# Kernel optimization log

Measured on AMD Instinct MI355X. Metric: run time of the kernel, lower is better.

Reference implementation:

```python
import jax, jax.numpy as jnp
import numpy as np

N = 50000   # total residue nodes across the batch of peptides
E = 800000  # total directed intra-peptide edges (avg degree 16)
D = 512


def _w(k, shape):
    fan_in = shape[0]
    return (jax.random.normal(k, shape, jnp.float32) / np.sqrt(fan_in)).astype(jnp.float32)


def setup_inputs() -> dict:
    key = jax.random.key(0)
    ks = jax.random.split(key, 12)
    return {
        "peptide_feature": jax.random.normal(ks[0], (N, D), jnp.float32),
        "edge_index": jax.random.randint(ks[1], (2, E), 0, N),
        # aanet_proj: 512 -> 1024 -> 1024 -> 512 -> 80 (ReLU between, none after last)
        "W1": _w(ks[2], (512, 1024)), "b1": jnp.zeros((1024,), jnp.float32),
        "W2": _w(ks[3], (1024, 1024)), "b2": jnp.zeros((1024,), jnp.float32),
        "W3": _w(ks[4], (1024, 512)), "b3": jnp.zeros((512,), jnp.float32),
        "W4": _w(ks[5], (512, 80)), "b4": jnp.zeros((80,), jnp.float32),
        # in_net: 80 -> 512
        "Win": _w(ks[6], (80, 512)), "bin_": jnp.zeros((512,), jnp.float32),
        # GIN conv MLP: 512 -> 512 -> 512 (eps = 0)
        "Wg1": _w(ks[7], (512, 512)), "bg1": jnp.zeros((512,), jnp.float32),
        "Wg2": _w(ks[8], (512, 512)), "bg2": jnp.zeros((512,), jnp.float32),
        # out_net: 512 -> 80
        "Wout": _w(ks[9], (512, 80)), "bout": jnp.zeros((80,), jnp.float32),
    }


def reference(peptide_feature, edge_index, W1, b1, W2, b2, W3, b3, W4, b4,
              Win, bin_, Wg1, bg1, Wg2, bg2, Wout, bout):
    relu = jax.nn.relu
    # aanet_proj
    h = relu(peptide_feature @ W1 + b1)
    h = relu(h @ W2 + b2)
    h = relu(h @ W3 + b3)
    peptide_feat = h @ W4 + b4                      # [N, 80]
    # in_net
    x = peptide_feat @ Win + bin_                   # [N, 512]
    # GIN message passing (sum aggregation, eps=0): per-sample loop in the
    # original is equivalent to one global pass since edges are sample-local.
    src, dst = edge_index[0], edge_index[1]
    agg = jax.ops.segment_sum(x[src], dst, num_segments=N)   # [N, 512]
    g = x + agg
    g = relu(g @ Wg1 + bg1) @ Wg2 + bg2             # GIN MLP
    # out_net
    peptide_mask = g @ Wout + bout                  # [N, 80]
    return peptide_mask, peptide_feat
```

## Files before the change

kernel.cpp:

```cpp
#include <hip/hip_runtime.h>
#include <stdint.h>


using bf16x8 = __attribute__((ext_vector_type(8))) short;
using f32x4  = __attribute__((ext_vector_type(4))) float;

__device__ inline unsigned short f2bf(float f) {
    union { float f; unsigned u; } v; v.f = f;
    unsigned u = v.u;
    u += 0x7FFFu + ((u >> 16) & 1u);
    return (unsigned short)(u >> 16);
}
__device__ inline float bf2f(unsigned u16) {
    return __uint_as_float(u16 << 16);
}

struct PreDescs {
    const float* W[8]; unsigned short* Wt[8];
    int K[8], M[8], Kp[8], ntx[8], start[8];
    int tEnd, cEnd, eEnd;
    const float* feat; unsigned short* featb; int nFeat;
    const int* ei; int E; int* cnt;
};

__global__ __launch_bounds__(256) void rg_preprocess(PreDescs d) {
    int b = blockIdx.x;
    int tid = threadIdx.x;
    if (b < d.tEnd) {
        __shared__ float t[32][33];
        int di = 0;
#pragma unroll
        for (int i = 1; i < 8; ++i) if (b >= d.start[i]) di = i;
        int local = b - d.start[di];
        int bx = local % d.ntx[di];
        int by = local / d.ntx[di];
        const float* W = d.W[di];
        unsigned short* Wt = d.Wt[di];
        int K = d.K[di], M = d.M[di], Kp = d.Kp[di];
        int mb = bx * 32, kb = by * 32;
        int tx = tid & 31, tg = tid >> 5;
#pragma unroll
        for (int p = 0; p < 4; ++p) {
            int r = tg + p * 8;
            int k = kb + r, m = mb + tx;
            t[r][tx] = (k < K && m < M) ? W[(size_t)k * M + m] : 0.f;
        }
        __syncthreads();
#pragma unroll
        for (int p = 0; p < 4; ++p) {
            int r = tg + p * 8;
            int mo = mb + r, ko = kb + tx;
            Wt[(size_t)mo * Kp + ko] = f2bf(t[tx][r]);
        }
    } else if (b < d.cEnd) {
        int i = ((b - d.tEnd) * 256 + tid) * 4;
        if (i + 3 < d.nFeat) {
            float4 v = *(const float4*)(d.feat + i);
            ushort4 o; o.x = f2bf(v.x); o.y = f2bf(v.y); o.z = f2bf(v.z); o.w = f2bf(v.w);
            *(ushort4*)(d.featb + i) = o;
        }
    } else {
        int e = (b - d.cEnd) * 256 + tid;
        if (e < d.E) atomicAdd(&d.cnt[d.ei[d.E + e]], 1);
    }
}

template <bool RELU, bool OUT_BF, bool OUT_F32, bool DEGB, int MT>
__device__ __forceinline__ void gemm_body(
    int bid,
    const unsigned short* __restrict__ A, const unsigned short* __restrict__ Bt,
    const float* __restrict__ bias, const int* __restrict__ deg, int Mvalid,
    unsigned short* __restrict__ outB, float* __restrict__ outF,
    int Nrows, int Kp, int Mp, int gN)
{
    __shared__ __align__(16) unsigned short As[128 * 64];
    __shared__ __align__(16) unsigned short Bs[128 * 64];

    int xcd = bid & 7;
    int slot = bid >> 3;
    int c = slot % MT;
    int rsub = slot / MT;
    int rt = rsub * 8 + xcd;
    if (rt >= gN) return;
    const int rowBase = rt * 128;
    const int nBase   = c * 128;

    const int tid  = threadIdx.x;
    const int lane = tid & 63;
    const int w    = tid >> 6;
    const int wm   = w & 1, wn = w >> 1;

    f32x4 acc[4][4];
#pragma unroll
    for (int i = 0; i < 4; ++i)
#pragma unroll
        for (int j = 0; j < 4; ++j) acc[i][j] = (f32x4){0.f, 0.f, 0.f, 0.f};

    const int nkt = Kp >> 6;
    for (int kt = 0; kt < nkt; ++kt) {
        __syncthreads();
        const int k0 = kt * 64;
#pragma unroll
        for (int i = 0; i < 4; ++i) {
            int q   = i * 256 + tid;
            int r   = q >> 3;
            int cbg = (q & 7) ^ (r & 7);
            const unsigned short* gp = A + (size_t)(rowBase + r) * Kp + k0 + cbg * 8;
            __builtin_amdgcn_global_load_lds(
                (const __attribute__((address_space(1))) void*)gp,
                (__attribute__((address_space(3))) void*)(&As[q * 8]), 16, 0, 0);
        }
#pragma unroll
        for (int i = 0; i < 4; ++i) {
            int q   = i * 256 + tid;
            int r   = q >> 3;
            int cbg = (q & 7) ^ (r & 7);
            const unsigned short* gp = Bt + (size_t)(nBase + r) * Kp + k0 + cbg * 8;
            __builtin_amdgcn_global_load_lds(
                (const __attribute__((address_space(1))) void*)gp,
                (__attribute__((address_space(3))) void*)(&Bs[q * 8]), 16, 0, 0);
        }
        __syncthreads();
#pragma unroll
        for (int kk = 0; kk < 2; ++kk) {
            bf16x8 a[4], b[4];
            const int cb = kk * 4 + (lane >> 4);
#pragma unroll
            for (int i = 0; i < 4; ++i) {
                int r = wm * 64 + i * 16 + (lane & 15);
                a[i] = *(const bf16x8*)&As[(r * 8 + (cb ^ (r & 7))) * 8];
            }
#pragma unroll
            for (int j = 0; j < 4; ++j) {
                int r = wn * 64 + j * 16 + (lane & 15);
                b[j] = *(const bf16x8*)&Bs[(r * 8 + (cb ^ (r & 7))) * 8];
            }
#pragma unroll
            for (int i = 0; i < 4; ++i)
#pragma unroll
                for (int j = 0; j < 4; ++j)
                    acc[i][j] = __builtin_amdgcn_mfma_f32_16x16x32_bf16(b[j], a[i], acc[i][j], 0, 0, 0);
        }
    }

    const int quad = lane >> 4;
#pragma unroll
    for (int i = 0; i < 4; ++i) {
        int row = rowBase + wm * 64 + i * 16 + (lane & 15);
        if (row >= Nrows) continue;
        float sc = 1.f;
        if (DEGB) sc = 1.f + (float)deg[row];
#pragma unroll
        for (int j = 0; j < 4; ++j) {
            int colb = nBase + wn * 64 + j * 16 + quad * 4;
            float4 bv = (colb < Mvalid) ? *(const float4*)(bias + colb)
                                        : (float4){0.f, 0.f, 0.f, 0.f};
            float v0 = acc[i][j][0] + sc * bv.x;
            float v1 = acc[i][j][1] + sc * bv.y;
            float v2 = acc[i][j][2] + sc * bv.z;
            float v3 = acc[i][j][3] + sc * bv.w;
            if (RELU) {
                v0 = v0 > 0.f ? v0 : 0.f; v1 = v1 > 0.f ? v1 : 0.f;
                v2 = v2 > 0.f ? v2 : 0.f; v3 = v3 > 0.f ? v3 : 0.f;
            }
            if (OUT_BF) {
                ushort4 o; o.x = f2bf(v0); o.y = f2bf(v1); o.z = f2bf(v2); o.w = f2bf(v3);
                *(ushort4*)(outB + (size_t)row * Mp + colb) = o;
            }
            if (OUT_F32) {
                if (colb < Mvalid)
                    *(float4*)(outF + (size_t)row * Mvalid + colb) = (float4){v0, v1, v2, v3};
            }
        }
    }
}

template <bool RELU, bool OUT_BF, bool OUT_F32, bool DEGB, int MT>
__global__ __launch_bounds__(256) void rg_gemm(
    const unsigned short* __restrict__ A, const unsigned short* __restrict__ Bt,
    const float* __restrict__ bias, const int* __restrict__ deg, int Mvalid,
    unsigned short* __restrict__ outB, float* __restrict__ outF,
    int Nrows, int Kp, int Mp, int gN)
{
    gemm_body<RELU, OUT_BF, OUT_F32, DEGB, MT>(blockIdx.x, A, Bt, bias, deg,
                                               Mvalid, outB, outF, Nrows, Kp, Mp, gN);
}

template <bool RELU, int MT>
__device__ __forceinline__ void gemm256_body(
    int bid,
    const unsigned short* __restrict__ A, const unsigned short* __restrict__ Bt,
    const float* __restrict__ bias, unsigned short* __restrict__ outB,
    int Nrows, int NrowsPad, int Kp, int Mp, int gN2)
{
    __shared__ __align__(16) unsigned short As[2][2][128 * 64];
    __shared__ __align__(16) unsigned short Bs[2][2][128 * 64];

    int xcd = bid & 7;
    int slotb = bid >> 3;
    int c = slotb % MT;
    int rsub = slotb / MT;
    int rt = rsub * 8 + xcd;
    if (rt >= gN2) return;
    const int rowBase = rt * 256;
    const int nBase   = c * 256;

    const int tid  = threadIdx.x;
    const int lane = tid & 63;
    const int w    = tid >> 6;
    const int wm   = w & 1;
    const int wn   = w >> 1;

    f32x4 acc[8][4];
#pragma unroll
    for (int i = 0; i < 8; ++i)
#pragma unroll
        for (int j = 0; j < 4; ++j) acc[i][j] = (f32x4){0.f, 0.f, 0.f, 0.f};

    const int nkt = Kp >> 6;

    auto stageA = [&](int t, int hf) {
        const int k0 = t << 6;
        unsigned short* dst = &As[t & 1][hf][0];
#pragma unroll
        for (int ld = 0; ld < 2; ++ld) {
            int q   = ld * 512 + tid;
            int r   = q >> 3;
            int cbg = (q & 7) ^ (r & 7);
            int grow = rowBase + hf * 128 + r;
            grow = grow < NrowsPad ? grow : NrowsPad - 1;
            const unsigned short* gp = A + (size_t)grow * Kp + k0 + cbg * 8;
            __builtin_amdgcn_global_load_lds(
                (const __attribute__((address_space(1))) void*)gp,
                (__attribute__((address_space(3))) void*)(dst + q * 8), 16, 0, 0);
        }
    };
    auto stageB = [&](int t, int hf) {
        const int k0 = t << 6;
        unsigned short* dst = &Bs[t & 1][hf][0];
#pragma unroll
        for (int ld = 0; ld < 2; ++ld) {
            int q   = ld * 512 + tid;
            int r   = q >> 3;
            int cbg = (q & 7) ^ (r & 7);
            const unsigned short* gp = Bt + (size_t)(nBase + hf * 128 + r) * Kp + k0 + cbg * 8;
            __builtin_amdgcn_global_load_lds(
                (const __attribute__((address_space(1))) void*)gp,
                (__attribute__((address_space(3))) void*)(dst + q * 8), 16, 0, 0);
        }
    };

    auto phase = [&](int a, int q, int mh, int nh) {
        const int slot = a & 1;
        bf16x8 av[4][2], bv[2][2];
#pragma unroll
        for (int i = 0; i < 4; ++i) {
            int lr = wm * 64 + i * 16 + (lane & 15);
#pragma unroll
            for (int kk = 0; kk < 2; ++kk) {
                int cb = kk * 4 + (lane >> 4);
                av[i][kk] = *(const bf16x8*)&As[slot][mh][(lr * 8 + (cb ^ (lr & 7))) * 8];
            }
        }
#pragma unroll
        for (int j = 0; j < 2; ++j) {
            int lr = wn * 32 + j * 16 + (lane & 15);
#pragma unroll
            for (int kk = 0; kk < 2; ++kk) {
                int cb = kk * 4 + (lane >> 4);
                bv[j][kk] = *(const bf16x8*)&Bs[slot][nh][(lr * 8 + (cb ^ (lr & 7))) * 8];
            }
        }
        if (q == 0) { if (a + 1 < nkt) stageA(a + 1, 1); }
        if (q == 1) { if (a + 1 < nkt) stageB(a + 1, 1); }
        if (q == 2) { if (a + 2 < nkt) stageA(a + 2, 0); }
        if (q == 3) {
            if (a + 2 < nkt) {
                stageB(a + 2, 0);
                asm volatile("s_waitcnt vmcnt(4)" ::: "memory");
            } else if (a + 1 < nkt) {
                asm volatile("s_waitcnt vmcnt(0)" ::: "memory");
            }
        }
        __builtin_amdgcn_sched_barrier(0);
        __builtin_amdgcn_s_barrier();
        asm volatile("s_waitcnt lgkmcnt(0)" ::: "memory");
        __builtin_amdgcn_sched_barrier(0);
        __builtin_amdgcn_s_setprio(1);
#pragma unroll
        for (int i = 0; i < 4; ++i)
#pragma unroll
            for (int j = 0; j < 2; ++j)
#pragma unroll
                for (int kk = 0; kk < 2; ++kk)
                    acc[mh * 4 + i][nh * 2 + j] = __builtin_amdgcn_mfma_f32_16x16x32_bf16(
                        bv[j][kk], av[i][kk], acc[mh * 4 + i][nh * 2 + j], 0, 0, 0);
        __builtin_amdgcn_s_setprio(0);
        __builtin_amdgcn_sched_barrier(0);
        __builtin_amdgcn_s_barrier();
    };

    stageA(0, 0); stageB(0, 0); stageA(0, 1); stageB(0, 1);
    stageA(1, 0); stageB(1, 0);
    asm volatile("s_waitcnt vmcnt(4)" ::: "memory");
    __builtin_amdgcn_sched_barrier(0);
    __builtin_amdgcn_s_barrier();
    __builtin_amdgcn_sched_barrier(0);

    for (int a = 0; a < nkt; ++a) {
        phase(a, 0, 0, 0);
        phase(a, 1, 0, 1);
        phase(a, 2, 1, 0);
        phase(a, 3, 1, 1);
    }

    const int quad = lane >> 4;
#pragma unroll
    for (int mi = 0; mi < 8; ++mi) {
        int row = rowBase + ((mi >> 2) * 2 + wm) * 64 + (mi & 3) * 16 + (lane & 15);
        if (row >= Nrows) continue;
#pragma unroll
        for (int nj = 0; nj < 4; ++nj) {
            int colb = nBase + (nj >> 1) * 128 + wn * 32 + (nj & 1) * 16 + quad * 4;
            float4 bvv = *(const float4*)(bias + colb);
            float v0 = acc[mi][nj][0] + bvv.x;
            float v1 = acc[mi][nj][1] + bvv.y;
            float v2 = acc[mi][nj][2] + bvv.z;
            float v3 = acc[mi][nj][3] + bvv.w;
            if (RELU) {
                v0 = v0 > 0.f ? v0 : 0.f; v1 = v1 > 0.f ? v1 : 0.f;
                v2 = v2 > 0.f ? v2 : 0.f; v3 = v3 > 0.f ? v3 : 0.f;
            }
            ushort4 o; o.x = f2bf(v0); o.y = f2bf(v1); o.z = f2bf(v2); o.w = f2bf(v3);
            *(ushort4*)(outB + (size_t)row * Mp + colb) = o;
        }
    }
}

template <bool RELU, int MT>
__global__ __launch_bounds__(512) void rg_gemm256(
    const unsigned short* __restrict__ A, const unsigned short* __restrict__ Bt,
    const float* __restrict__ bias, unsigned short* __restrict__ outB,
    int Nrows, int NrowsPad, int Kp, int Mp, int gN2)
{
    gemm256_body<RELU, MT>(blockIdx.x, A, Bt, bias, outB, Nrows, NrowsPad, Kp, Mp, gN2);
}

__global__ __launch_bounds__(512) void rg_gemm256_l1_scatter(
    const unsigned short* __restrict__ A, const unsigned short* __restrict__ Bt,
    const float* __restrict__ bias, unsigned short* __restrict__ outB,
    int Nrows, int NrowsPad, int Kp, int Mp, int gN2,
    int gemmBlocks, const int* __restrict__ ei, int E,
    int* __restrict__ cursor, int* __restrict__ cols)
{
    int bid = blockIdx.x;
    if (bid < gemmBlocks) {
        gemm256_body<true, 4>(bid, A, Bt, bias, outB, Nrows, NrowsPad, Kp, Mp, gN2);
    } else {
        int e = (bid - gemmBlocks) * 512 + threadIdx.x;
        if (e < E) {
            int d = ei[E + e];
            int p = atomicAdd(&cursor[d], 1);
            cols[p] = ei[e];
        }
    }
}

__device__ __forceinline__ void rg_gridbar(int* bar, int nb, int phase) {
    __syncthreads();
    if (threadIdx.x == 0) {
        __threadfence();
        atomicAdd(bar, 1);
        int target = phase * nb;
        while (__hip_atomic_load(bar, __ATOMIC_RELAXED, __HIP_MEMORY_SCOPE_AGENT) < target) {}
        __threadfence();
    }
    __syncthreads();
}

__global__ __launch_bounds__(1024) void rg_scan_all(
    const int* __restrict__ cnt, int* __restrict__ rowptr, int* __restrict__ cursor,
    int* __restrict__ bsums, int* bar, int Nn, int E, int nb)
{
    __shared__ int sd[1024];
    const int tid = threadIdx.x;
    const int bid = blockIdx.x;
    const int i   = bid * 1024 + tid;

    int v = (i < Nn) ? cnt[i] : 0;
    sd[tid] = v;
    __syncthreads();
    for (int off = 1; off < 1024; off <<= 1) {
        int t = (tid >= off) ? sd[tid - off] : 0;
        __syncthreads();
        sd[tid] += t;
        __syncthreads();
    }
    if (tid == 1023) bsums[bid] = sd[1023];
    rg_gridbar(bar, nb, 1);

    if (bid == 0 && tid < 64) {
        int bv = (tid < nb) ? bsums[tid] : 0;
        int incl = bv;
#pragma unroll
        for (int off = 1; off < 64; off <<= 1) {
            int t = __shfl_up(incl, off, 64);
            if (tid >= off) incl += t;
        }
        if (tid < nb) bsums[tid] = incl - bv;
    }
    rg_gridbar(bar, nb, 2);

    if (i < Nn) {
        int ex = sd[tid] - v + bsums[bid];
        rowptr[i] = ex; cursor[i] = ex;
    }
    if (i == 0) rowptr[Nn] = E;
}

__global__ __launch_bounds__(256) void rg_agg80(
    const unsigned short* __restrict__ pf, const int* __restrict__ rowptr,
    const int* __restrict__ cols, unsigned short* __restrict__ s, int Nn)
{
    int node = blockIdx.x * 4 + (threadIdx.x >> 6);
    if (node >= Nn) return;
    int lane = threadIdx.x & 63;
    const unsigned* xp = (const unsigned*)pf;
    size_t off = (size_t)node * 64 + lane;
    unsigned u = xp[off];
    float a0 = bf2f(u & 0xffffu), a1 = bf2f(u >> 16);
    int beg = rowptr[node], end = rowptr[node + 1];
    int e = beg;
    for (; e + 8 <= end; e += 8) {
        unsigned v[8];
#pragma unroll
        for (int t = 0; t < 8; ++t) v[t] = xp[(size_t)cols[e + t] * 64 + lane];
#pragma unroll
        for (int t = 0; t < 8; ++t) { a0 += bf2f(v[t] & 0xffffu); a1 += bf2f(v[t] >> 16); }
    }
    for (; e < end; ++e) {
        unsigned v = xp[(size_t)cols[e] * 64 + lane];
        a0 += bf2f(v & 0xffffu); a1 += bf2f(v >> 16);
    }
    unsigned o = (unsigned)f2bf(a0) | ((unsigned)f2bf(a1) << 16);
    ((unsigned*)s)[off] = o;
}

extern "C" void kernel_launch(void* const* d_in, const int* in_sizes, int n_in,
                              void* d_out, int out_size, void* d_ws, size_t ws_size,
                              hipStream_t stream)
{
    const float* feat = (const float*)d_in[0];
    const int*   ei   = (const int*)d_in[1];
    const float* W1 = (const float*)d_in[2];  const float* b1 = (const float*)d_in[3];
    const float* W2 = (const float*)d_in[4];  const float* b2 = (const float*)d_in[5];
    const float* W3 = (const float*)d_in[6];  const float* b3 = (const float*)d_in[7];
    const float* W4 = (const float*)d_in[8];  const float* b4 = (const float*)d_in[9];
    const float* Wi = (const float*)d_in[10]; const float* bi = (const float*)d_in[11];
    const float* Wg1 = (const float*)d_in[12]; const float* bg1 = (const float*)d_in[13];
    const float* Wg2 = (const float*)d_in[14]; const float* bg2 = (const float*)d_in[15];
    const float* Wo = (const float*)d_in[16]; const float* bo = (const float*)d_in[17];

    const int N = in_sizes[0] / 512;
    const int E = in_sizes[1] / 2;
    const int gN = (N + 127) / 128;
    const int Npad = gN * 128;

    char* ws = (char*)d_ws;
    size_t o = 0;
    auto alloc = [&](size_t bytes) { char* p = ws + o; o += (bytes + 255) & ~(size_t)255; return p; };
    unsigned short* bufA = (unsigned short*)alloc((size_t)Npad * 1024 * 2);
    unsigned short* bufB = (unsigned short*)alloc((size_t)Npad * 1024 * 2);
    unsigned short* bufC = (unsigned short*)alloc((size_t)Npad * 512 * 2);
    unsigned short* W1t = (unsigned short*)alloc((size_t)1024 * 512 * 2);
    unsigned short* W2t = (unsigned short*)alloc((size_t)1024 * 1024 * 2);
    unsigned short* W3t = (unsigned short*)alloc((size_t)512 * 1024 * 2);
    unsigned short* W4t = (unsigned short*)alloc((size_t)128 * 512 * 2);
    unsigned short* Wit = (unsigned short*)alloc((size_t)512 * 128 * 2);
    unsigned short* Wg1t = (unsigned short*)alloc((size_t)512 * 512 * 2);
    unsigned short* Wg2t = (unsigned short*)alloc((size_t)512 * 512 * 2);
    unsigned short* Wot = (unsigned short*)alloc((size_t)128 * 512 * 2);
    int* cnt    = (int*)alloc((size_t)(N + 64) * 4);
    int* bar    = cnt + N;
    int* rowptr = (int*)alloc((size_t)(N + 1) * 4);
    int* cursor = (int*)alloc((size_t)N * 4);
    int* cols   = (int*)alloc((size_t)E * 4);
    int* bsums  = (int*)alloc(256);

    float* out_mask = (float*)d_out;
    float* out_feat = (float*)d_out + (size_t)N * 80;

    hipMemsetAsync(cnt, 0, (size_t)(N + 64) * 4, stream);
    {
        PreDescs d;
        const float* Ws[8]  = {W1, W2, W3, W4, Wi, Wg1, Wg2, Wo};
        unsigned short* Ts[8] = {W1t, W2t, W3t, W4t, Wit, Wg1t, Wg2t, Wot};
        int Ks[8]  = {512, 1024, 1024, 512, 80, 512, 512, 512};
        int Ms[8]  = {1024, 1024, 512, 80, 512, 512, 512, 80};
        int Kps[8] = {512, 1024, 1024, 512, 128, 512, 512, 512};
        int Mps[8] = {1024, 1024, 512, 128, 512, 512, 512, 128};
        int st = 0;
        for (int i = 0; i < 8; ++i) {
            d.W[i] = Ws[i]; d.Wt[i] = Ts[i];
            d.K[i] = Ks[i]; d.M[i] = Ms[i]; d.Kp[i] = Kps[i];
            d.ntx[i] = Mps[i] / 32;
            d.start[i] = st;
            st += (Mps[i] / 32) * (Kps[i] / 32);
        }
        d.tEnd = st;
        d.cEnd = st + (N * 512) / 1024;
        d.eEnd = d.cEnd + (E + 255) / 256;
        d.feat = feat; d.featb = bufC; d.nFeat = N * 512;
        d.ei = ei; d.E = E; d.cnt = cnt;
        rg_preprocess<<<d.eEnd, 256, 0, stream>>>(d);
    }

    const int nb = (N + 1023) / 1024;
    rg_scan_all<<<nb, 1024, 0, stream>>>(cnt, rowptr, cursor, bsums, bar, N, E, nb);

    const int rg8 = ((gN + 7) / 8) * 8;
    auto grid = [&](int MT) { return dim3(rg8 * MT); };
    const int gN2 = (N + 255) / 256;
    const int rg256 = ((gN2 + 7) / 8) * 8;

    {
        const int gemmBlocks = rg256 * 4;
        const int scatBlocks = (E + 511) / 512;
        rg_gemm256_l1_scatter<<<dim3(gemmBlocks + scatBlocks), 512, 0, stream>>>(
            bufC, W1t, b1, bufA, N, Npad, 512, 1024, gN2,
            gemmBlocks, ei, E, cursor, cols);
    }

    rg_gemm256<true, 4><<<dim3(rg256 * 4), 512, 0, stream>>>(bufA, W2t, b2, bufB, N, Npad, 1024, 1024, gN2);
    rg_gemm256<true, 2><<<dim3(rg256 * 2), 512, 0, stream>>>(bufB, W3t, b3, bufC, N, Npad, 1024, 512, gN2);
    rg_gemm<false, true, true, false, 1><<<grid(1), 256, 0, stream>>>(bufC, W4t, b4, nullptr, 80, bufA, out_feat, N, 512, 128, gN);

    rg_agg80<<<(N + 3) / 4, 256, 0, stream>>>(bufA, rowptr, cols, bufC, N);

    rg_gemm<false, true, false, true, 4><<<grid(4), 256, 0, stream>>>(bufC, Wit, bi, cnt, 512, bufA, nullptr, N, 128, 512, gN);
    rg_gemm256<true, 2><<<dim3(rg256 * 2), 512, 0, stream>>>(bufA, Wg1t, bg1, bufB, N, Npad, 512, 512, gN2);
    rg_gemm256<false, 2><<<dim3(rg256 * 2), 512, 0, stream>>>(bufB, Wg2t, bg2, bufC, N, Npad, 512, 512, gN2);
    rg_gemm<false, false, true, false, 1><<<grid(1), 256, 0, stream>>>(bufC, Wot, bo, nullptr, 80, nullptr, out_mask, N, 512, 128, gN);
}
```

Before: 847.5 us.

## Merge GEMM k-tile phases from four to two and keep B fragments in registers

The inner k-tile loop of the 256x256 bf16 MFMA GEMM now runs two phases instead of four. All B fragments for a k-tile are loaded from LDS once, in the first phase, and reused across both M halves. Prefetches are grouped so A and B stage together, which halves the number of barriers and waitcnt points per k-tile. A min-occupancy hint is also added to launch_bounds. Holding B across phases raises register pressure, and the occupancy hint may cap VGPRs enough to cause spills given the 128-float accumulator.

After: 786.5 us. 7.2% less time.

```diff
diff --git a/kernel.cpp b/kernel.cpp
--- a/kernel.cpp
+++ b/kernel.cpp
@@ -210,6 +210,8 @@
     const int w    = tid >> 6;
     const int wm   = w & 1;
     const int wn   = w >> 1;
+    const int lane15 = lane & 15;
+    const int laneq  = lane >> 4;
 
     f32x4 acc[8][4];
 #pragma unroll
@@ -250,33 +252,36 @@
         }
     };
 
-    auto phase = [&](int a, int q, int mh, int nh) {
+    bf16x8 av[4][2];
+    bf16x8 bv[2][2][2];
+
+    auto phase = [&](int a, int ph) {
         const int slot = a & 1;
-        bf16x8 av[4][2], bv[2][2];
 #pragma unroll
         for (int i = 0; i < 4; ++i) {
-            int lr = wm * 64 + i * 16 + (lane & 15);
+            int lr = wm * 64 + i * 16 + lane15;
 #pragma unroll
             for (int kk = 0; kk < 2; ++kk) {
-                int cb = kk * 4 + (lane >> 4);
-                av[i][kk] = *(const bf16x8*)&As[slot][mh][(lr * 8 + (cb ^ (lr & 7))) * 8];
-            }
-        }
-#pragma unroll
-        for (int j = 0; j < 2; ++j) {
-            int lr = wn * 32 + j * 16 + (lane & 15);
-#pragma unroll
-            for (int kk = 0; kk < 2; ++kk) {
-                int cb = kk * 4 + (lane >> 4);
-                bv[j][kk] = *(const bf16x8*)&Bs[slot][nh][(lr * 8 + (cb ^ (lr & 7))) * 8];
-            }
-        }
-        if (q == 0) { if (a + 1 < nkt) stageA(a + 1, 1); }
-        if (q == 1) { if (a + 1 < nkt) stageB(a + 1, 1); }
-        if (q == 2) { if (a + 2 < nkt) stageA(a + 2, 0); }
-        if (q == 3) {
+                int cb = kk * 4 + laneq;
+                av[i][kk] = *(const bf16x8*)&As[slot][ph][(lr * 8 + (cb ^ (lr & 7))) * 8];
+            }
+        }
+        if (ph == 0) {
+#pragma unroll
+            for (int nh = 0; nh < 2; ++nh)
+#pragma unroll
+                for (int j = 0; j < 2; ++j) {
+                    int lr = wn * 32 + j * 16 + lane15;
+#pragma unroll
+                    for (int kk = 0; kk < 2; ++kk) {
+                        int cb = kk * 4 + laneq;
+                        bv[nh][j][kk] = *(const bf16x8*)&Bs[slot][nh][(lr * 8 + (cb ^ (lr & 7))) * 8];
+                    }
+                }
+            if (a + 1 < nkt) { stageA(a + 1, 1); stageB(a + 1, 1); }
+        } else {
             if (a + 2 < nkt) {
-                stageB(a + 2, 0);
+                stageA(a + 2, 0); stageB(a + 2, 0);
                 asm volatile("s_waitcnt vmcnt(4)" ::: "memory");
             } else if (a + 1 < nkt) {
                 asm volatile("s_waitcnt vmcnt(0)" ::: "memory");
@@ -288,13 +293,15 @@
         __builtin_amdgcn_sched_barrier(0);
         __builtin_amdgcn_s_setprio(1);
 #pragma unroll
-        for (int i = 0; i < 4; ++i)
-#pragma unroll
-            for (int j = 0; j < 2; ++j)
-#pragma unroll
-                for (int kk = 0; kk < 2; ++kk)
-                    acc[mh * 4 + i][nh * 2 + j] = __builtin_amdgcn_mfma_f32_16x16x32_bf16(
-                        bv[j][kk], av[i][kk], acc[mh * 4 + i][nh * 2 + j], 0, 0, 0);
+        for (int nh = 0; nh < 2; ++nh)
+#pragma unroll
+            for (int i = 0; i < 4; ++i)
+#pragma unroll
+                for (int j = 0; j < 2; ++j)
+#pragma unroll
+                    for (int kk = 0; kk < 2; ++kk)
+                        acc[ph * 4 + i][nh * 2 + j] = __builtin_amdgcn_mfma_f32_16x16x32_bf16(
+                            bv[nh][j][kk], av[i][kk], acc[ph * 4 + i][nh * 2 + j], 0, 0, 0);
         __builtin_amdgcn_s_setprio(0);
         __builtin_amdgcn_sched_barrier(0);
         __builtin_amdgcn_s_barrier();
@@ -308,10 +315,8 @@
     __builtin_amdgcn_sched_barrier(0);
 
     for (int a = 0; a < nkt; ++a) {
-        phase(a, 0, 0, 0);
-        phase(a, 1, 0, 1);
-        phase(a, 2, 1, 0);
-        phase(a, 3, 1, 1);
+        phase(a, 0);
+        phase(a, 1);
     }
 
     const int quad = lane >> 4;
@@ -338,7 +343,7 @@
 }
 
 template <bool RELU, int MT>
-__global__ __launch_bounds__(512) void rg_gemm256(
+__global__ __launch_bounds__(512, 2) void rg_gemm256(
     const unsigned short* __restrict__ A, const unsigned short* __restrict__ Bt,
     const float* __restrict__ bias, unsigned short* __restrict__ outB,
     int Nrows, int NrowsPad, int Kp, int Mp, int gN2)
@@ -346,7 +351,7 @@
     gemm256_body<RELU, MT>(blockIdx.x, A, Bt, bias, outB, Nrows, NrowsPad, Kp, Mp, gN2);
 }
 
-__global__ __launch_bounds__(512) void rg_gemm256_l1_scatter(
+__global__ __launch_bounds__(512, 2) void rg_gemm256_l1_scatter(
     const unsigned short* __restrict__ A, const unsigned short* __restrict__ Bt,
     const float* __restrict__ bias, unsigned short* __restrict__ outB,
     int Nrows, int NrowsPad, int Kp, int Mp, int gN2,
```
